# Kernel optimization log

Measured on AMD Instinct MI355X. Metric: run time of the kernel, lower is better.

Reference implementation:

```python
import jax, jax.numpy as jnp
import numpy as np

DIM = 768
HEADS = 12
HEAD_DIM = DIM // HEADS
SCALE = HEAD_DIM ** -0.5
ALPHA = 0.1


def setup_inputs() -> dict:
    key = jax.random.key(0)
    ks = jax.random.split(key, 6)
    B, N, C = 16, 577, DIM
    x = jax.random.normal(ks[0], (B, N, C), dtype=jnp.float32)
    attn_weight = jax.random.uniform(ks[1], (B, N - 1), dtype=jnp.float32)
    w_qkv = jax.random.normal(ks[2], (C, 3 * C), dtype=jnp.float32) * (C ** -0.5)
    b_qkv = jnp.zeros((3 * C,), dtype=jnp.float32)
    w_proj = jax.random.normal(ks[3], (C, C), dtype=jnp.float32) * (C ** -0.5)
    b_proj = jnp.zeros((C,), dtype=jnp.float32)
    return {"x": x, "attn_weight": attn_weight, "w_qkv": w_qkv, "b_qkv": b_qkv,
            "w_proj": w_proj, "b_proj": b_proj}


def reference(x, attn_weight, w_qkv, b_qkv, w_proj, b_proj):
    B, N, C = x.shape
    H, D = HEADS, HEAD_DIM
    qkv = (x @ w_qkv + b_qkv).reshape(B, N, 3, H, D)
    qkv = jnp.transpose(qkv, (2, 0, 3, 1, 4))  # [3, B, H, N, D]
    q, k, v = qkv[0], qkv[1], qkv[2]
    attn = jnp.einsum('bhnd,bhmd->bhnm', q, k) * SCALE  # [B,H,N,N]
    patch_attn = attn[:, :, 0, 1:]  # pre-softmax CLS->patch scores
    # reweight CLS row (excluding CLS->CLS) before softmax
    w = attn_weight[:, None, None, :]  # [B,1,1,N-1]
    cls_row = attn[:, :, 0:1, 1:] * (w * ALPHA + (1.0 - ALPHA))
    attn = attn.at[:, :, 0:1, 1:].set(cls_row)
    attn = jax.nn.softmax(attn, axis=-1)
    out = jnp.einsum('bhnm,bhmd->bhnd', attn, v)
    out = jnp.transpose(out, (0, 2, 1, 3)).reshape(B, N, C)
    out = out @ w_proj + b_proj
    return out, patch_attn
```

## Files before the change

### kernel.cpp

```cpp
#include <hip/hip_runtime.h>
#include <hip/hip_bf16.h>
#include <math.h>

#define B_    16
#define N_    577
#define C_    768
#define H_    12
#define D_    64
#define M_    (B_ * N_)
#define MP_   9344
#define QKVN  2304
#define NP_   640
#define SCALE 0.125f
#define ALPHA 0.1f
#define OUT0  (B_ * N_ * C_)

#define NB_CONV 7008
#define NB_T1   1728
#define NB_T2   576

typedef __attribute__((ext_vector_type(8))) short short8;
typedef __attribute__((ext_vector_type(4))) float f32x4;
typedef __hip_bfloat16 bf16;

__device__ __forceinline__ float exp2fast(float x) {
    return __builtin_amdgcn_exp2f(x);
}

__device__ __forceinline__ void load16(const void* g, void* l) {
    __builtin_amdgcn_global_load_lds(
        (const __attribute__((address_space(1))) unsigned int*)g,
        (__attribute__((address_space(3))) unsigned int*)l, 16, 0, 0);
}

__device__ __forceinline__ f32x4 mfma16(short8 a, short8 b, f32x4 c) {
    return __builtin_amdgcn_mfma_f32_16x16x32_bf16(a, b, c, 0, 0, 0);
}

__global__ __launch_bounds__(256) void prep(const float* __restrict__ x,
                                            bf16* __restrict__ xb,
                                            const float* __restrict__ wq,
                                            bf16* __restrict__ wqT,
                                            const float* __restrict__ wp,
                                            bf16* __restrict__ wpT) {
    __shared__ float tile[32][33];
    const int bid = blockIdx.x;
    if (bid < NB_CONV) {
        int idx = bid * 256 + threadIdx.x;
        int m = idx / 192;
        bf16 tmp[4];
        if (m < M_) {
            float4 f = ((const float4*)x)[idx];
            tmp[0] = __float2bfloat16(f.x);
            tmp[1] = __float2bfloat16(f.y);
            tmp[2] = __float2bfloat16(f.z);
            tmp[3] = __float2bfloat16(f.w);
        } else {
            tmp[0] = tmp[1] = tmp[2] = tmp[3] = __float2bfloat16(0.f);
        }
        ((ushort4*)xb)[idx] = *(ushort4*)tmp;
        return;
    }
    const float* src; bf16* dst; int C, R, bx, by;
    if (bid < NB_CONV + NB_T1) {
        int r = bid - NB_CONV;
        bx = r % 72; by = r / 72; src = wq; dst = wqT; R = 768; C = QKVN;
    } else {
        int r = bid - NB_CONV - NB_T1;
        bx = r % 24; by = r / 24; src = wp; dst = wpT; R = 768; C = 768;
    }
    int cb = bx * 32, rb = by * 32;
    int tx = threadIdx.x & 31, ty = threadIdx.x >> 5;
    #pragma unroll
    for (int i = 0; i < 32; i += 8)
        tile[ty + i][tx] = src[(size_t)(rb + ty + i) * C + cb + tx];
    __syncthreads();
    #pragma unroll
    for (int i = 0; i < 32; i += 8)
        dst[(size_t)(cb + ty + i) * R + rb + tx] = __float2bfloat16(tile[tx][ty + i]);
}

__global__ __launch_bounds__(256) void gemm_bt(const bf16* __restrict__ A,
                                               const bf16* __restrict__ BT,
                                               const float* __restrict__ bias,
                                               bf16* __restrict__ q,
                                               bf16* __restrict__ kk,
                                               bf16* __restrict__ vt,
                                               float* __restrict__ out,
                                               int mode, int nby) {
    __shared__ __align__(16) char smem[35840];
    bf16* Tt = (bf16*)smem;

    const int L = blockIdx.x;
    const int xcd = L & 7;
    const int li = L >> 3;
    const int mi = li % 10;
    const int nb = li / 10;
    const int slab = (xcd == 0) ? 10 : 9;
    if (mi >= slab) return;
    const int mb = (xcd == 0) ? mi : (10 + (xcd - 1) * 9 + mi);

    const int m0 = mb * 128, n0 = nb * 128;
    const int t = threadIdx.x, lane = t & 63, w = t >> 6;
    const int wr = w >> 1, wc = w & 1;
    const int rsel = lane & 15, ksel = (lane >> 4) * 8;
    const int r16 = lane & 15, quad = lane >> 4;

    f32x4 acc[4][4];
    #pragma unroll
    for (int i = 0; i < 4; i++)
        #pragma unroll
        for (int j = 0; j < 4; j++) acc[i][j] = (f32x4)(0.f);

    const int srow = w * 32 + (lane >> 2);
    const int scol = (lane & 3) * 8;
    const bf16* ga = A  + (size_t)(m0 + srow) * 768 + scol;
    const bf16* gb = BT + (size_t)(n0 + srow) * 768 + scol;

    auto stage = [&](int kt, int buf) {
        bf16* dstA = (bf16*)(smem + buf * 16384);
        bf16* dstB = dstA + 4096;
        int gc = kt * 32;
        load16(ga + gc,            dstA + (w * 32) * 32);
        load16(ga + gc + 16 * 768, dstA + (w * 32 + 16) * 32);
        load16(gb + gc,            dstB + (w * 32) * 32);
        load16(gb + gc + 16 * 768, dstB + (w * 32 + 16) * 32);
    };

    stage(0, 0);
    __syncthreads();

    for (int kt = 0; kt < 24; kt++) {
        const int cur = kt & 1;
        if (kt < 23) stage(kt + 1, cur ^ 1);

        const bf16* As = (const bf16*)(smem + cur * 16384);
        const bf16* Bs = As + 4096;
        short8 af[4], bfg[4];
        #pragma unroll
        for (int mi2 = 0; mi2 < 4; mi2++)
            af[mi2] = *(const short8*)(As + (wr * 64 + mi2 * 16 + rsel) * 32 + ksel);
        #pragma unroll
        for (int nj = 0; nj < 4; nj++)
            bfg[nj] = *(const short8*)(Bs + (wc * 64 + nj * 16 + rsel) * 32 + ksel);
        #pragma unroll
        for (int mi2 = 0; mi2 < 4; mi2++)
            #pragma unroll
            for (int nj = 0; nj < 4; nj++)
                acc[mi2][nj] = mfma16(af[mi2], bfg[nj], acc[mi2][nj]);
        __syncthreads();
    }

    float bs[4];
    #pragma unroll
    for (int nj = 0; nj < 4; nj++) bs[nj] = bias[n0 + wc * 64 + nj * 16 + r16];

    if (mode == 1) {
        const int row0 = quad * 4;
        #pragma unroll
        for (int mi2 = 0; mi2 < 4; mi2++) {
            #pragma unroll
            for (int nj = 0; nj < 4; nj++) {
                #pragma unroll
                for (int r = 0; r < 4; r++) {
                    int m = m0 + wr * 64 + mi2 * 16 + row0 + r;
                    if (m >= M_) continue;
                    int cc = n0 + wc * 64 + nj * 16 + r16;
                    out[(size_t)m * 768 + cc] = acc[mi2][nj][r] + bs[nj];
                }
            }
        }
        return;
    }

    #pragma unroll
    for (int mi2 = 0; mi2 < 4; mi2++) {
        #pragma unroll
        for (int nj = 0; nj < 4; nj++) {
            bf16 pk[4];
            #pragma unroll
            for (int r = 0; r < 4; r++)
                pk[r] = __float2bfloat16(acc[mi2][nj][r] + bs[nj]);
            int ccl = wc * 64 + nj * 16 + r16;
            int ml4 = wr * 64 + mi2 * 16 + quad * 4;
            *(uint2*)&Tt[ccl * 140 + ml4] = *(const uint2*)pk;
        }
    }
    __syncthreads();

    const int part = nb / 6;
    if (part < 2) {
        int nl = t & 127, half = t >> 7;
        int m = m0 + nl;
        if (m < M_) {
            int b = m / N_, n = m - b * N_;
            int h = (nb % 6) * 2 + half;
            bf16* dst = (part == 0 ? q : kk) + ((size_t)(b * H_ + h) * N_ + n) * 64;
            #pragma unroll
            for (int d8 = 0; d8 < 8; d8++) {
                bf16 tv[8];
                #pragma unroll
                for (int dd = 0; dd < 8; dd++)
                    tv[dd] = Tt[(half * 64 + d8 * 8 + dd) * 140 + nl];
                *(uint4*)(dst + d8 * 8) = *(const uint4*)tv;
            }
        }
    } else {
        int dr = t >> 1, seg = t & 1;
        int rem = (nb % 6) * 128 + dr;
        int h = rem >> 6, d = rem & 63;
        int mb2 = m0 + seg * 64;
        int b = mb2 / N_;
        int n = mb2 - b * N_;
        const bf16* src = Tt + dr * 140 + seg * 64;
        int i = 0;
        while (i < 64 && mb2 + i < M_) {
            if (n == N_) { b++; n = 0; }
            bf16* drow = vt + ((size_t)(b * H_ + h) * 64 + d) * NP_;
            if ((n & 7) == 0 && n + 8 <= N_ && i + 8 <= 64 && mb2 + i + 8 <= M_) {
                bf16 tv[8];
                #pragma unroll
                for (int dd = 0; dd < 8; dd++) tv[dd] = src[i + dd];
                *(uint4*)(drow + n) = *(const uint4*)tv;
                i += 8; n += 8;
            } else {
                drow[n] = src[i]; i++; n++;
            }
        }
    }
}

__global__ __launch_bounds__(256) void attn_mfma(const bf16* __restrict__ q,
                                                 const bf16* __restrict__ k,
                                                 const bf16* __restrict__ vt,
                                                 const float* __restrict__ aw,
                                                 bf16* __restrict__ ao,
                                                 float* __restrict__ patch) {
    __shared__ bf16 Kb[2][4096];
    __shared__ bf16 Vb[2][4096];
    __shared__ bf16 Pb[4][2048];
    const int bh = blockIdx.x, qt = blockIdx.y;
    const int b = bh / H_, h = bh - b * H_;
    const int t = threadIdx.x, lane = t & 63, w = t >> 6;
    const int r16 = lane & 15, quad = lane >> 4;
    const float SC2 = SCALE * 1.44269504f;

    const bf16* kbp = k + (size_t)bh * N_ * 64;
    const bf16* vbp = vt + (size_t)bh * 64 * NP_;

    short8 qa0[2], qa1[2];
    #pragma unroll
    for (int mi = 0; mi < 2; mi++) {
        int qrow = qt * 128 + w * 32 + mi * 16 + r16;
        int qrc = (qrow < N_) ? qrow : (N_ - 1);
        const bf16* qp = q + ((size_t)bh * N_ + qrc) * 64 + quad * 8;
        qa0[mi] = *(const short8*)(qp);
        qa1[mi] = *(const short8*)(qp + 32);
    }

    f32x4 Oacc[2][4];
    #pragma unroll
    for (int mi = 0; mi < 2; mi++)
        #pragma unroll
        for (int d0 = 0; d0 < 4; d0++) Oacc[mi][d0] = (f32x4)(0.f);
    float lrow[2][4];
    #pragma unroll
    for (int mi = 0; mi < 2; mi++)
        #pragma unroll
        for (int rr = 0; rr < 4; rr++) lrow[mi][rr] = 0.f;

    const bool clsrow = (qt == 0) && (w == 0) && (quad == 0);

    auto stage = [&](int kt, int buf) {
        #pragma unroll
        for (int is = 0; is < 2; is++) {
            int base = is * 256 + w * 64;
            int slot = base + lane;
            int row = slot >> 3, pos = slot & 7;
            int c = pos ^ (row & 7);
            int jg = kt * 64 + row; if (jg > N_ - 1) jg = N_ - 1;
            load16(kbp + (size_t)jg * 64 + c * 8, &Kb[buf][base * 8]);
        }
        #pragma unroll
        for (int is = 0; is < 2; is++) {
            int base = is * 256 + w * 64;
            int slot = base + lane;
            int row = slot >> 3, pos = slot & 7;
            int c = pos ^ (row & 7);
            load16(vbp + (size_t)row * NP_ + kt * 64 + c * 8, &Vb[buf][base * 8]);
        }
    };

    stage(0, 0);
    __syncthreads();

    for (int kt = 0; kt < 10; kt++) {
        const int cur = kt & 1;
        if (kt < 9) stage(kt + 1, cur ^ 1);

        f32x4 S[2][4];
        #pragma unroll
        for (int j0 = 0; j0 < 4; j0++) {
            int row = j0 * 16 + r16;
            const bf16* kpl = &Kb[cur][row * 64];
            short8 kf0 = *(const short8*)(kpl + ((quad ^ (row & 7)) << 3));
            short8 kf1 = *(const short8*)(kpl + (((quad ^ 4) ^ (row & 7)) << 3));
            #pragma unroll
            for (int mi = 0; mi < 2; mi++) {
                f32x4 sa = (f32x4)(0.f);
                sa = mfma16(qa0[mi], kf0, sa);
                sa = mfma16(qa1[mi], kf1, sa);
                S[mi][j0] = sa;
            }
        }

        if (kt < 9) {
            #pragma unroll
            for (int mi = 0; mi < 2; mi++) {
                #pragma unroll
                for (int j0 = 0; j0 < 4; j0++) {
                    float wfac = 1.f;
                    if (mi == 0 && clsrow) {
                        int c = kt * 64 + j0 * 16 + r16;
                        if (c >= 1) {
                            patch[(size_t)bh * (N_ - 1) + (c - 1)] = S[0][j0][0] * SCALE;
                            wfac = aw[b * (N_ - 1) + (c - 1)] * ALPHA + (1.f - ALPHA);
                        }
                    }
                    #pragma unroll
                    for (int rr = 0; rr < 4; rr++) {
                        float v = S[mi][j0][rr] * SC2;
                        if (rr == 0) v *= wfac;
                        float p = exp2fast(v);
                        S[mi][j0][rr] = p;
                        lrow[mi][rr] += p;
                    }
                }
            }
        } else {
            #pragma unroll
            for (int mi = 0; mi < 2; mi++) {
                #pragma unroll
                for (int j0 = 0; j0 < 4; j0++) {
                    int c = kt * 64 + j0 * 16 + r16;
                    bool valid = (c < N_);
                    float wfac = 1.f;
                    if (mi == 0 && clsrow && valid) {
                        patch[(size_t)bh * (N_ - 1) + (c - 1)] = S[0][j0][0] * SCALE;
                        wfac = aw[b * (N_ - 1) + (c - 1)] * ALPHA + (1.f - ALPHA);
                    }
                    #pragma unroll
                    for (int rr = 0; rr < 4; rr++) {
                        float v = S[mi][j0][rr] * SC2;
                        if (rr == 0) v *= wfac;
                        float p = valid ? exp2fast(v) : 0.f;
                        S[mi][j0][rr] = p;
                        lrow[mi][rr] += p;
                    }
                }
            }
        }

        bf16* pw = &Pb[w][0];
        #pragma unroll
        for (int mi = 0; mi < 2; mi++) {
            #pragma unroll
            for (int j0 = 0; j0 < 4; j0++) {
                int cg = j0 * 2 + (r16 >> 3);
                #pragma unroll
                for (int rr = 0; rr < 4; rr++) {
                    int rp = mi * 16 + quad * 4 + rr;
                    pw[rp * 64 + ((cg ^ (rp & 7)) << 3) + (r16 & 7)] =
                        __float2bfloat16(S[mi][j0][rr]);
                }
            }
        }
        short8 pa0[2], pa1[2];
        #pragma unroll
        for (int mi = 0; mi < 2; mi++) {
            int rp = mi * 16 + r16;
            const bf16* pr = pw + rp * 64;
            pa0[mi] = *(const short8*)(pr + ((quad ^ (rp & 7)) << 3));
            pa1[mi] = *(const short8*)(pr + (((quad ^ 4) ^ (rp & 7)) << 3));
        }

        #pragma unroll
        for (int d0 = 0; d0 < 4; d0++) {
            int row = d0 * 16 + r16;
            const bf16* vpl = &Vb[cur][row * 64];
            short8 vf0 = *(const short8*)(vpl + ((quad ^ (row & 7)) << 3));
            short8 vf1 = *(const short8*)(vpl + (((quad ^ 4) ^ (row & 7)) << 3));
            #pragma unroll
            for (int mi = 0; mi < 2; mi++) {
                Oacc[mi][d0] = mfma16(pa0[mi], vf0, Oacc[mi][d0]);
                Oacc[mi][d0] = mfma16(pa1[mi], vf1, Oacc[mi][d0]);
            }
        }
        __syncthreads();
    }

    #pragma unroll
    for (int mi = 0; mi < 2; mi++) {
        #pragma unroll
        for (int rr = 0; rr < 4; rr++) {
            float l = lrow[mi][rr];
            l += __shfl_xor(l, 1);
            l += __shfl_xor(l, 2);
            l += __shfl_xor(l, 4);
            l += __shfl_xor(l, 8);
            int n = qt * 128 + w * 32 + mi * 16 + quad * 4 + rr;
            if (n >= N_) continue;
            float inv = 1.f / l;
            #pragma unroll
            for (int d0 = 0; d0 < 4; d0++) {
                ao[((size_t)(b * N_ + n) * H_ + h) * 64 + d0 * 16 + r16] =
                    __float2bfloat16(Oacc[mi][d0][rr] * inv);
            }
        }
    }
}

extern "C" void kernel_launch(void* const* d_in, const int* in_sizes, int n_in,
                              void* d_out, int out_size, void* d_ws, size_t ws_size,
                              hipStream_t stream) {
    const float* x      = (const float*)d_in[0];
    const float* aw     = (const float*)d_in[1];
    const float* w_qkv  = (const float*)d_in[2];
    const float* b_qkv  = (const float*)d_in[3];
    const float* w_proj = (const float*)d_in[4];
    const float* b_proj = (const float*)d_in[5];
    float* out = (float*)d_out;

    char* ws = (char*)d_ws;
    bf16* xbf    = (bf16*)(ws);
    bf16* wqkvT  = (bf16*)(ws + 14352384);
    bf16* wprojT = (bf16*)(ws + 17891328);
    bf16* qv     = (bf16*)(ws + 19070976);
    bf16* kv     = (bf16*)(ws + 33251328);
    bf16* vt     = (bf16*)(ws + 47431680);
    bf16* ao     = xbf;

    prep<<<NB_CONV + NB_T1 + NB_T2, 256, 0, stream>>>(x, xbf, w_qkv, wqkvT, w_proj, wprojT);

    gemm_bt<<<8 * 10 * 18, 256, 0, stream>>>(
        xbf, wqkvT, b_qkv, qv, kv, vt, nullptr, 0, 18);

    attn_mfma<<<dim3(H_ * B_, 5), 256, 0, stream>>>(qv, kv, vt, aw, ao, out + OUT0);

    gemm_bt<<<8 * 10 * 6, 256, 0, stream>>>(
        ao, wprojT, b_proj, nullptr, nullptr, nullptr, out, 1, 6);
}
```

Baseline: 225.8 us.

## Replace direct global-to-LDS loads with register-staged prefetch and swizzle epilogue tile

```diff
diff --git a/kernel.cpp b/kernel.cpp
--- a/kernel.cpp
+++ b/kernel.cpp
@@ -19,18 +19,14 @@
 #define NB_T1   1728
 #define NB_T2   576
 
+#define TT(cc, m) (((cc) << 7) + ((((m) >> 2) ^ ((cc) & 31)) << 2) + ((m) & 3))
+
 typedef __attribute__((ext_vector_type(8))) short short8;
 typedef __attribute__((ext_vector_type(4))) float f32x4;
 typedef __hip_bfloat16 bf16;
 
 __device__ __forceinline__ float exp2fast(float x) {
     return __builtin_amdgcn_exp2f(x);
-}
-
-__device__ __forceinline__ void load16(const void* g, void* l) {
-    __builtin_amdgcn_global_load_lds(
-        (const __attribute__((address_space(1))) unsigned int*)g,
-        (__attribute__((address_space(3))) unsigned int*)l, 16, 0, 0);
 }
 
 __device__ __forceinline__ f32x4 mfma16(short8 a, short8 b, f32x4 c) {
@@ -88,7 +84,7 @@
                                                bf16* __restrict__ vt,
                                                float* __restrict__ out,
                                                int mode, int nby) {
-    __shared__ __align__(16) char smem[35840];
+    __shared__ __align__(16) char smem[32768];
     bf16* Tt = (bf16*)smem;
 
     const int L = blockIdx.x;
@@ -116,25 +112,26 @@
     const int scol = (lane & 3) * 8;
     const bf16* ga = A  + (size_t)(m0 + srow) * 768 + scol;
     const bf16* gb = BT + (size_t)(n0 + srow) * 768 + scol;
-
-    auto stage = [&](int kt, int buf) {
+    const int loff = w * 1024 + lane * 8;
+
+    uint4 ra0[2], ra1[2], rb0[2], rb1[2];
+    auto fetch = [&](int kt, int s) {
+        int gc = kt * 32;
+        ra0[s] = *(const uint4*)(ga + gc);
+        ra1[s] = *(const uint4*)(ga + gc + 16 * 768);
+        rb0[s] = *(const uint4*)(gb + gc);
+        rb1[s] = *(const uint4*)(gb + gc + 16 * 768);
+    };
+    auto commit = [&](int s, int buf) {
         bf16* dstA = (bf16*)(smem + buf * 16384);
         bf16* dstB = dstA + 4096;
-        int gc = kt * 32;
-        load16(ga + gc,            dstA + (w * 32) * 32);
-        load16(ga + gc + 16 * 768, dstA + (w * 32 + 16) * 32);
-        load16(gb + gc,            dstB + (w * 32) * 32);
-        load16(gb + gc + 16 * 768, dstB + (w * 32 + 16) * 32);
+        *(uint4*)(dstA + loff)       = ra0[s];
+        *(uint4*)(dstA + loff + 512) = ra1[s];
+        *(uint4*)(dstB + loff)       = rb0[s];
+        *(uint4*)(dstB + loff + 512) = rb1[s];
     };
-
-    stage(0, 0);
-    __syncthreads();
-
-    for (int kt = 0; kt < 24; kt++) {
-        const int cur = kt & 1;
-        if (kt < 23) stage(kt + 1, cur ^ 1);
-
-        const bf16* As = (const bf16*)(smem + cur * 16384);
+    auto compute = [&](int buf) {
+        const bf16* As = (const bf16*)(smem + buf * 16384);
         const bf16* Bs = As + 4096;
         short8 af[4], bfg[4];
         #pragma unroll
@@ -148,6 +145,22 @@
             #pragma unroll
             for (int nj = 0; nj < 4; nj++)
                 acc[mi2][nj] = mfma16(af[mi2], bfg[nj], acc[mi2][nj]);
+    };
+
+    fetch(0, 0);
+    fetch(1, 1);
+    commit(0, 0);
+    __syncthreads();
+
+    for (int ktp = 0; ktp < 12; ktp++) {
+        const int kt0 = 2 * ktp;
+        if (kt0 + 2 < 24) fetch(kt0 + 2, 0);
+        compute(0);
+        commit(1, 1);
+        __syncthreads();
+        if (kt0 + 3 < 24) fetch(kt0 + 3, 1);
+        compute(1);
+        if (kt0 + 2 < 24) commit(0, 0);
         __syncthreads();
     }
 
@@ -183,7 +196,7 @@
                 pk[r] = __float2bfloat16(acc[mi2][nj][r] + bs[nj]);
             int ccl = wc * 64 + nj * 16 + r16;
             int ml4 = wr * 64 + mi2 * 16 + quad * 4;
-            *(uint2*)&Tt[ccl * 140 + ml4] = *(const uint2*)pk;
+            *(uint2*)&Tt[TT(ccl, ml4)] = *(const uint2*)pk;
         }
     }
     __syncthreads();
@@ -201,7 +214,7 @@
                 bf16 tv[8];
                 #pragma unroll
                 for (int dd = 0; dd < 8; dd++)
-                    tv[dd] = Tt[(half * 64 + d8 * 8 + dd) * 140 + nl];
+                    tv[dd] = Tt[TT(half * 64 + d8 * 8 + dd, nl)];
                 *(uint4*)(dst + d8 * 8) = *(const uint4*)tv;
             }
         }
@@ -212,19 +225,19 @@
         int mb2 = m0 + seg * 64;
         int b = mb2 / N_;
         int n = mb2 - b * N_;
-        const bf16* src = Tt + dr * 140 + seg * 64;
         int i = 0;
         while (i < 64 && mb2 + i < M_) {
             if (n == N_) { b++; n = 0; }
             bf16* drow = vt + ((size_t)(b * H_ + h) * 64 + d) * NP_;
+            int m = seg * 64 + i;
             if ((n & 7) == 0 && n + 8 <= N_ && i + 8 <= 64 && mb2 + i + 8 <= M_) {
                 bf16 tv[8];
                 #pragma unroll
-                for (int dd = 0; dd < 8; dd++) tv[dd] = src[i + dd];
+                for (int dd = 0; dd < 8; dd++) tv[dd] = Tt[TT(dr, m + dd)];
                 *(uint4*)(drow + n) = *(const uint4*)tv;
                 i += 8; n += 8;
             } else {
-                drow[n] = src[i]; i++; n++;
+                drow[n] = Tt[TT(dr, m)]; i++; n++;
             }
         }
     }
@@ -271,32 +284,32 @@
 
     const bool clsrow = (qt == 0) && (w == 0) && (quad == 0);
 
-    auto stage = [&](int kt, int buf) {
-        #pragma unroll
-        for (int is = 0; is < 2; is++) {
-            int base = is * 256 + w * 64;
-            int slot = base + lane;
-            int row = slot >> 3, pos = slot & 7;
-            int c = pos ^ (row & 7);
-            int jg = kt * 64 + row; if (jg > N_ - 1) jg = N_ - 1;
-            load16(kbp + (size_t)jg * 64 + c * 8, &Kb[buf][base * 8]);
-        }
-        #pragma unroll
-        for (int is = 0; is < 2; is++) {
-            int base = is * 256 + w * 64;
-            int slot = base + lane;
-            int row = slot >> 3, pos = slot & 7;
-            int c = pos ^ (row & 7);
-            load16(vbp + (size_t)row * NP_ + kt * 64 + c * 8, &Vb[buf][base * 8]);
-        }
+    uint4 rk0, rk1, rv0, rv1;
+    auto fetchKV = [&](int kt) {
+        int s0 = w * 64 + lane, s1 = 256 + w * 64 + lane;
+        int row0 = s0 >> 3, c0 = (s0 & 7) ^ (row0 & 7);
+        int row1 = s1 >> 3, c1 = (s1 & 7) ^ (row1 & 7);
+        int jg0 = kt * 64 + row0; if (jg0 > N_ - 1) jg0 = N_ - 1;
+        int jg1 = kt * 64 + row1; if (jg1 > N_ - 1) jg1 = N_ - 1;
+        rk0 = *(const uint4*)(kbp + (size_t)jg0 * 64 + c0 * 8);
+        rk1 = *(const uint4*)(kbp + (size_t)jg1 * 64 + c1 * 8);
+        rv0 = *(const uint4*)(vbp + (size_t)row0 * NP_ + kt * 64 + c0 * 8);
+        rv1 = *(const uint4*)(vbp + (size_t)row1 * NP_ + kt * 64 + c1 * 8);
     };
-
-    stage(0, 0);
+    auto commitKV = [&](int buf) {
+        *(uint4*)(&Kb[buf][(w * 64) * 8 + lane * 8])       = rk0;
+        *(uint4*)(&Kb[buf][(256 + w * 64) * 8 + lane * 8]) = rk1;
+        *(uint4*)(&Vb[buf][(w * 64) * 8 + lane * 8])       = rv0;
+        *(uint4*)(&Vb[buf][(256 + w * 64) * 8 + lane * 8]) = rv1;
+    };
+
+    fetchKV(0);
+    commitKV(0);
     __syncthreads();
 
     for (int kt = 0; kt < 10; kt++) {
         const int cur = kt & 1;
-        if (kt < 9) stage(kt + 1, cur ^ 1);
+        if (kt < 9) fetchKV(kt + 1);
 
         f32x4 S[2][4];
         #pragma unroll
@@ -396,6 +409,8 @@
                 Oacc[mi][d0] = mfma16(pa1[mi], vf1, Oacc[mi][d0]);
             }
         }
+
+        if (kt < 9) commitKV(cur ^ 1);
         __syncthreads();
     }
 
```

New measurement: 374.7 us. 65.9% more time.
